# Optimization experiments

Hardware: AMD Instinct MI355X
Metric: run time of the kernel (lower is better)

## Reference

```python
import jax, jax.numpy as jnp
import numpy as np
import math

B, S, DIM, H = 4, 1024, 4096, 32
HD = DIM // H  # head_dim = 128
MAX_B, MAX_S = 4, 1024
START_POS = 0
ROPE_THETA = 10000.0


def setup_inputs() -> dict:
    key = jax.random.key(0)
    ks = jax.random.split(key, 6)
    x = jax.random.normal(ks[0], (B, S, DIM), dtype=jnp.float32)
    # real RoPE frequencies: freqs_cis[t, j] = exp(i * t * theta^{-2j/hd})
    inv_freq = 1.0 / (ROPE_THETA ** (jnp.arange(0, HD, 2, dtype=jnp.float32) / HD))  # [HD/2]
    t = jnp.arange(START_POS, START_POS + S, dtype=jnp.float32)
    ang = jnp.outer(t, inv_freq)  # [S, HD/2]
    freqs_cos = jnp.cos(ang)
    freqs_sin = jnp.sin(ang)
    # additive causal mask as in llama: -inf above diagonal offset start_pos+1
    mask = jnp.triu(jnp.full((1, 1, S, S), float('-inf'), dtype=jnp.float32), k=START_POS + 1)
    scale = 0.02
    wq = jax.random.normal(ks[1], (DIM, DIM), dtype=jnp.float32) * scale
    wk = jax.random.normal(ks[2], (DIM, DIM), dtype=jnp.float32) * scale
    wv = jax.random.normal(ks[3], (DIM, DIM), dtype=jnp.float32) * scale
    wo = jax.random.normal(ks[4], (DIM, DIM), dtype=jnp.float32) * scale
    cache_k = jnp.zeros((MAX_B, MAX_S, H, HD), dtype=jnp.float32)
    cache_v = jnp.zeros((MAX_B, MAX_S, H, HD), dtype=jnp.float32)
    return {"x": x, "start_pos": START_POS, "freqs_cos": freqs_cos, "freqs_sin": freqs_sin,
            "mask": mask, "wq": wq, "wk": wk, "wv": wv, "wo": wo,
            "cache_k": cache_k, "cache_v": cache_v}


def _apply_rotary(t, cos, sin):
    # t: [B, S, H, HD]; interpret last dim as HD/2 complex pairs (real, imag)
    b, s, h, d = t.shape
    tr = t.reshape(b, s, h, d // 2, 2)
    a, bb = tr[..., 0], tr[..., 1]
    c = cos[None, :, None, :]  # [1, S, 1, HD/2]
    si = sin[None, :, None, :]
    out_r = a * c - bb * si
    out_i = a * si + bb * c
    return jnp.stack([out_r, out_i], axis=-1).reshape(b, s, h, d)


def reference(x, start_pos, freqs_cos, freqs_sin, mask, wq, wk, wv, wo, cache_k, cache_v):
    bsz, seqlen, dim = x.shape
    hd = HD
    # torch Linear: y = x @ W.T, W is [out, in]
    xq = (x @ wq.T).reshape(bsz, seqlen, H, hd)
    xk = (x @ wk.T).reshape(bsz, seqlen, H, hd)
    xv = (x @ wv.T).reshape(bsz, seqlen, H, hd)
    xq = _apply_rotary(xq, freqs_cos, freqs_sin)
    xk = _apply_rotary(xk, freqs_cos, freqs_sin)
    # KV-cache write
    cache_k = jax.lax.dynamic_update_slice(cache_k, xk, (0, start_pos, 0, 0))
    cache_v = jax.lax.dynamic_update_slice(cache_v, xv, (0, start_pos, 0, 0))
    keys = cache_k[:bsz, :start_pos + seqlen]    # [B, K, H, HD]
    values = cache_v[:bsz, :start_pos + seqlen]  # [B, K, H, HD]
    # naive attention: full score matrix
    scores = jnp.einsum('bqhd,bkhd->bhqk', xq, keys) / math.sqrt(hd)
    scores = scores + mask
    probs = jax.nn.softmax(scores.astype(jnp.float32), axis=-1).astype(xq.dtype)
    out = jnp.einsum('bhqk,bkhd->bqhd', probs, values)
    out = out.reshape(bsz, seqlen, -1)
    return out @ wo.T
```

## Files before the change

### kernel.cpp

```cpp
#include <hip/hip_runtime.h>
#include <hip/hip_bf16.h>
#include <cstdint>

typedef __hip_bfloat16 bf16;
typedef __attribute__((ext_vector_type(8))) short frag8;
typedef __attribute__((ext_vector_type(4))) float f32x4;

#define DEV __device__ __forceinline__

DEV void gl_lds16(const void* g, void* l) {
  __builtin_amdgcn_global_load_lds(
      (const __attribute__((address_space(1))) void*)g,
      (__attribute__((address_space(3))) void*)l, 16, 0, 0);
}

DEV void storeC(float* C, size_t idx, float v) { C[idx] = v; }
DEV void storeC(bf16* C, size_t idx, float v) { C[idx] = __float2bfloat16(v); }

__global__ __launch_bounds__(256) void conv_kernel(const float* __restrict__ in,
                                                   bf16* __restrict__ out, int n8) {
  int i = blockIdx.x * 256 + threadIdx.x;
  if (i >= n8) return;
  const float4* in4 = reinterpret_cast<const float4*>(in);
  float4 a = in4[2 * i], b = in4[2 * i + 1];
  union { frag8 v; bf16 h[8]; } u;
  u.h[0] = __float2bfloat16(a.x); u.h[1] = __float2bfloat16(a.y);
  u.h[2] = __float2bfloat16(a.z); u.h[3] = __float2bfloat16(a.w);
  u.h[4] = __float2bfloat16(b.x); u.h[5] = __float2bfloat16(b.y);
  u.h[6] = __float2bfloat16(b.z); u.h[7] = __float2bfloat16(b.w);
  *reinterpret_cast<frag8*>(out + (size_t)i * 8) = u.v;
}

#define MF(a, b, c) __builtin_amdgcn_mfma_f32_16x16x32_bf16(a, b, c, 0, 0, 0)

#define STAGE(isB, h, tt, bp) do {                                             \
    char* _d = lds + ((isB) * 65536) + ((((bp) * 2) + (h)) << 14);             \
    gl_lds16(((isB) ? gB : gA)[h][0] + (size_t)(tt) * 64, _d + ldsOff0);       \
    gl_lds16(((isB) ? gB : gA)[h][1] + (size_t)(tt) * 64, _d + ldsOff1);       \
  } while (0)

#define RDA(mi, ckk) (*(const frag8*)(ab + aRowB + (mi) * 2048 + (ckk)))
#define RDB(ni, ckk) (*(const frag8*)(bb + bRowB + (ni) * 2048 + (ckk)))

#define PHASE(p, SSTAGE, SWAIT) do {                                           \
    if ((p) == 0) {                                                            \
      b00 = RDB(0, ck0); b01 = RDB(0, ck1); b10 = RDB(1, ck0); b11 = RDB(1, ck1); \
      b20 = RDB(2, ck0); b21 = RDB(2, ck1); b30 = RDB(3, ck0); b31 = RDB(3, ck1); \
    }                                                                          \
    frag8 a00 = RDA(2 * (p), ck0), a01 = RDA(2 * (p), ck1);                    \
    frag8 a10 = RDA(2 * (p) + 1, ck0), a11 = RDA(2 * (p) + 1, ck1);            \
    SSTAGE;                                                                    \
    SWAIT;                                                                     \
    __builtin_amdgcn_s_barrier();                                              \
    __builtin_amdgcn_s_setprio(1);                                             \
    acc[2*(p)][0]   = MF(a00, b00, acc[2*(p)][0]);                             \
    acc[2*(p)][1]   = MF(a00, b10, acc[2*(p)][1]);                             \
    acc[2*(p)][2]   = MF(a00, b20, acc[2*(p)][2]);                             \
    acc[2*(p)][3]   = MF(a00, b30, acc[2*(p)][3]);                             \
    acc[2*(p)+1][0] = MF(a10, b00, acc[2*(p)+1][0]);                           \
    acc[2*(p)+1][1] = MF(a10, b10, acc[2*(p)+1][1]);                           \
    acc[2*(p)+1][2] = MF(a10, b20, acc[2*(p)+1][2]);                           \
    acc[2*(p)+1][3] = MF(a10, b30, acc[2*(p)+1][3]);                           \
    acc[2*(p)][0]   = MF(a01, b01, acc[2*(p)][0]);                             \
    acc[2*(p)][1]   = MF(a01, b11, acc[2*(p)][1]);                             \
    acc[2*(p)][2]   = MF(a01, b21, acc[2*(p)][2]);                             \
    acc[2*(p)][3]   = MF(a01, b31, acc[2*(p)][3]);                             \
    acc[2*(p)+1][0] = MF(a11, b01, acc[2*(p)+1][0]);                           \
    acc[2*(p)+1][1] = MF(a11, b11, acc[2*(p)+1][1]);                           \
    acc[2*(p)+1][2] = MF(a11, b21, acc[2*(p)+1][2]);                           \
    acc[2*(p)+1][3] = MF(a11, b31, acc[2*(p)+1][3]);                           \
    __builtin_amdgcn_s_setprio(0);                                             \
    __builtin_amdgcn_s_barrier();                                              \
  } while (0)

#define VM4 asm volatile("s_waitcnt vmcnt(4)" ::: "memory")
#define VM0 asm volatile("s_waitcnt vmcnt(0)" ::: "memory")
#define NOW ((void)0)

#define TILE(t, SA, SB, SWAIT) do {                                            \
    const int _bp2 = ((t) & 1) * 2;                                            \
    char* ab = lds + ((_bp2 + wm) << 14);                                      \
    char* bb = lds + 65536 + ((_bp2 + bhalf) << 14);                           \
    PHASE(0, { if (SA) STAGE(0, 0, (t) + 1, ((t) + 1) & 1); }, NOW);           \
    PHASE(1, { if (SA) STAGE(0, 1, (t) + 1, ((t) + 1) & 1); }, NOW);           \
    PHASE(2, { if (SB) STAGE(1, 0, (t) + 2, (t) & 1); }, NOW);                 \
    PHASE(3, { if (SB) STAGE(1, 1, (t) + 2, (t) & 1); }, SWAIT);               \
  } while (0)

template <typename OutT>
__global__ __launch_bounds__(512, 2) void gemm8(const bf16* __restrict__ A,
                                                const bf16* __restrict__ Bt,
                                                OutT* __restrict__ C) {
  __shared__ __align__(16) char lds[131072];
  const int K = 4096, N = 4096;
  const int t = threadIdx.x;
  const int lane = t & 63, w = t >> 6;
  const int wm = w >> 2, wn = w & 3;
  const int lr = lane & 15, lg = lane >> 4;
  const int bhalf = wn >> 1;

  const int bid = blockIdx.x;
  const int wg = (bid & 7) * 32 + (bid >> 3);
  const int m0 = (wg >> 4) * 256, n0 = (wg & 15) * 256;

  const bf16* gA[2][2];
  const bf16* gB[2][2];
  int ldsOff0, ldsOff1;
  {
    int c0 = (w * 2 + 0) * 64 + lane;
    int c1 = (w * 2 + 1) * 64 + lane;
    int r0 = c0 >> 3, r1 = c1 >> 3;
    int e0 = ((c0 & 7) ^ (r0 & 7)) * 8;
    int e1 = ((c1 & 7) ^ (r1 & 7)) * 8;
    ldsOff0 = c0 * 16; ldsOff1 = c1 * 16;
    gA[0][0] = A + (size_t)(m0 + r0) * K + e0;
    gA[0][1] = A + (size_t)(m0 + r1) * K + e1;
    gA[1][0] = A + (size_t)(m0 + 128 + r0) * K + e0;
    gA[1][1] = A + (size_t)(m0 + 128 + r1) * K + e1;
    gB[0][0] = Bt + (size_t)(n0 + r0) * K + e0;
    gB[0][1] = Bt + (size_t)(n0 + r1) * K + e1;
    gB[1][0] = Bt + (size_t)(n0 + 128 + r0) * K + e0;
    gB[1][1] = Bt + (size_t)(n0 + 128 + r1) * K + e1;
  }

  const int swz = (lr & 7) << 4;
  const int ck0 = (lg * 16) ^ swz;
  const int ck1 = (64 + lg * 16) ^ swz;
  const int aRowB = lr * 128;
  const int bRowB = ((wn & 1) * 64 + lr) * 128;

  f32x4 acc[8][4];
#pragma unroll
  for (int mi = 0; mi < 8; ++mi)
#pragma unroll
    for (int ni = 0; ni < 4; ++ni) acc[mi][ni] = (f32x4){0.f, 0.f, 0.f, 0.f};

  frag8 b00, b01, b10, b11, b20, b21, b30, b31;

  STAGE(1, 0, 0, 0); STAGE(1, 1, 0, 0);
  STAGE(0, 0, 0, 0); STAGE(0, 1, 0, 0);
  STAGE(1, 0, 1, 1); STAGE(1, 1, 1, 1);
  VM4;
  __builtin_amdgcn_s_barrier();

  for (int tt = 0; tt < 62; tt += 2) {
    TILE(tt, 1, 1, VM4);
    TILE(tt + 1, 1, 1, VM4);
  }
  TILE(62, 1, 0, VM0);
  TILE(63, 0, 0, NOW);

#pragma unroll
  for (int mi = 0; mi < 8; ++mi)
#pragma unroll
    for (int ni = 0; ni < 4; ++ni) {
      f32x4 v = acc[mi][ni];
      int col = n0 + wn * 64 + ni * 16 + lr;
#pragma unroll
      for (int i = 0; i < 4; ++i) {
        int row = m0 + wm * 128 + mi * 16 + lg * 4 + i;
        storeC(C, (size_t)row * N + col, v[i]);
      }
    }
}

__global__ __launch_bounds__(256) void rope_kernel(bf16* __restrict__ q, bf16* __restrict__ k,
                                                   const float* __restrict__ fc,
                                                   const float* __restrict__ fs) {
  int idx = blockIdx.x * 256 + threadIdx.x;
  int i = idx & 63;
  int s = (idx >> 11) & 1023;
  float c = fc[s * 64 + i], sn = fs[s * 64 + i];
  uint32_t* qp = reinterpret_cast<uint32_t*>(q) + idx;
  uint32_t* kp = reinterpret_cast<uint32_t*>(k) + idx;
  union { uint32_t u; bf16 h[2]; } a, r;
  a.u = *qp;
  {
    float x = __bfloat162float(a.h[0]), y = __bfloat162float(a.h[1]);
    r.h[0] = __float2bfloat16(x * c - y * sn);
    r.h[1] = __float2bfloat16(x * sn + y * c);
    *qp = r.u;
  }
  a.u = *kp;
  {
    float x = __bfloat162float(a.h[0]), y = __bfloat162float(a.h[1]);
    r.h[0] = __float2bfloat16(x * c - y * sn);
    r.h[1] = __float2bfloat16(x * sn + y * c);
    *kp = r.u;
  }
}

__global__ __launch_bounds__(256) void transpose_v_kernel(const bf16* __restrict__ v,
                                                          bf16* __restrict__ vt) {
  __shared__ unsigned short tile[32][40];
  const int st = blockIdx.x * 32;
  const int dt = blockIdx.y * 32;
  const int bh = blockIdx.z;
  const int b = bh >> 5, h = bh & 31;
  const int t = threadIdx.x;
  const int r = t >> 3, c4 = (t & 7) * 4;
  const unsigned short* src = reinterpret_cast<const unsigned short*>(v) +
      ((size_t)(b * 1024 + st + r)) * 4096 + h * 128 + dt + c4;
  uint2 d = *reinterpret_cast<const uint2*>(src);
  tile[r][c4 + 0] = (unsigned short)(d.x & 0xffff);
  tile[r][c4 + 1] = (unsigned short)(d.x >> 16);
  tile[r][c4 + 2] = (unsigned short)(d.y & 0xffff);
  tile[r][c4 + 3] = (unsigned short)(d.y >> 16);
  __syncthreads();
  uint2 o;
  o.x = (uint32_t)tile[c4 + 0][r] | ((uint32_t)tile[c4 + 1][r] << 16);
  o.y = (uint32_t)tile[c4 + 2][r] | ((uint32_t)tile[c4 + 3][r] << 16);
  unsigned short* dst = reinterpret_cast<unsigned short*>(vt) +
      ((size_t)bh * 128 + dt + r) * 1024 + st + c4;
  *reinterpret_cast<uint2*>(dst) = o;
}

__global__ __launch_bounds__(256) void attn_kernel(const bf16* __restrict__ q,
                                                   const bf16* __restrict__ k,
                                                   const bf16* __restrict__ vt,
                                                   bf16* __restrict__ out) {
  __shared__ bf16 Kls[64 * 128];
  __shared__ bf16 Vls[128 * 64];
  __shared__ bf16 Pls[4][16 * 64];
  const int qt = blockIdx.x, h = blockIdx.y, b = blockIdx.z;
  const int t = threadIdx.x;
  const int lane = t & 63, wid = t >> 6;
  const int lr = lane & 15, lg = lane >> 4;

  frag8 aq[4];
  {
    const bf16* qp = q + ((size_t)(b * 1024 + qt * 64 + wid * 16 + lr)) * 4096 + h * 128 + lg * 8;
#pragma unroll
    for (int ks = 0; ks < 4; ++ks) aq[ks] = *reinterpret_cast<const frag8*>(qp + ks * 32);
  }

  const bf16* kbase = k + (size_t)b * 1024 * 4096 + h * 128;
  const bf16* vbase = vt + ((size_t)(b * 32 + h)) * 128 * 1024;
  const bf16* ksrc[4]; const bf16* vsrc[4]; char* kdst[4]; char* vdst[4];
#pragma unroll
  for (int c = 0; c < 4; ++c) {
    int L = t * 16 + c * 4096;
    int kr = L >> 8, kc = (L & 255) ^ ((kr & 7) << 4);
    ksrc[c] = kbase + (size_t)kr * 4096 + (kc >> 1);
    kdst[c] = (char*)Kls + L;
    int vr = L >> 7, vc = (L & 127) ^ ((vr & 7) << 4);
    vsrc[c] = vbase + (size_t)vr * 1024 + (vc >> 1);
    vdst[c] = (char*)Vls + L;
  }

  f32x4 oacc[8] = {};
  float mrow[4] = {-1e30f, -1e30f, -1e30f, -1e30f};
  float lrow[4] = {0.f, 0.f, 0.f, 0.f};
  char* Pw = (char*)&Pls[wid][0];
  const float scale = 0.08838834764831845f;

  for (int kt = 0; kt <= qt; ++kt) {
    __syncthreads();
#pragma unroll
    for (int c = 0; c < 4; ++c) {
      gl_lds16(ksrc[c] + (size_t)kt * 262144, kdst[c]);
      gl_lds16(vsrc[c] + kt * 64, vdst[c]);
    }
    __syncthreads();

    f32x4 sacc[4] = {};
#pragma unroll
    for (int ks = 0; ks < 4; ++ks) {
#pragma unroll
      for (int ni = 0; ni < 4; ++ni) {
        int n = ni * 16 + lr;
        frag8 bk = *reinterpret_cast<const frag8*>(
            (const char*)Kls + n * 256 + ((ks * 64 + lg * 16) ^ ((n & 7) << 4)));
        sacc[ni] = __builtin_amdgcn_mfma_f32_16x16x32_bf16(aq[ks], bk, sacc[ni], 0, 0, 0);
      }
    }

    float sv[4][4];
#pragma unroll
    for (int ni = 0; ni < 4; ++ni)
#pragma unroll
      for (int i = 0; i < 4; ++i) {
        float x = sacc[ni][i] * scale;
        if (kt == qt) {
          int qr = wid * 16 + lg * 4 + i;
          int kc = ni * 16 + lr;
          if (kc > qr) x = -1e30f;
        }
        sv[ni][i] = x;
      }

    float fs_[4];
#pragma unroll
    for (int i = 0; i < 4; ++i) {
      float pm = fmaxf(fmaxf(sv[0][i], sv[1][i]), fmaxf(sv[2][i], sv[3][i]));
#pragma unroll
      for (int m = 1; m <= 8; m <<= 1) pm = fmaxf(pm, __shfl_xor(pm, m));
      float mn = fmaxf(mrow[i], pm);
      float f = __expf(mrow[i] - mn);
      float rs = 0.f;
#pragma unroll
      for (int ni = 0; ni < 4; ++ni) {
        float p = __expf(sv[ni][i] - mn);
        sv[ni][i] = p;
        rs += p;
      }
#pragma unroll
      for (int m = 1; m <= 8; m <<= 1) rs += __shfl_xor(rs, m);
      lrow[i] = lrow[i] * f + rs;
      mrow[i] = mn;
      fs_[i] = f;
    }
#pragma unroll
    for (int nj = 0; nj < 8; ++nj)
#pragma unroll
      for (int i = 0; i < 4; ++i) oacc[nj][i] *= fs_[i];

#pragma unroll
    for (int ni = 0; ni < 4; ++ni)
#pragma unroll
      for (int i = 0; i < 4; ++i) {
        int prow = lg * 4 + i;
        int pb = prow * 128 + (((ni * 16 + lr) * 2) ^ ((prow & 7) << 4));
        *reinterpret_cast<bf16*>(Pw + pb) = __float2bfloat16(sv[ni][i]);
      }

#pragma unroll
    for (int ks2 = 0; ks2 < 2; ++ks2) {
      frag8 ap = *reinterpret_cast<const frag8*>(
          Pw + lr * 128 + ((ks2 * 64 + lg * 16) ^ ((lr & 7) << 4)));
#pragma unroll
      for (int nj = 0; nj < 8; ++nj) {
        int d = nj * 16 + lr;
        frag8 bv = *reinterpret_cast<const frag8*>(
            (const char*)Vls + d * 128 + ((ks2 * 64 + lg * 16) ^ ((d & 7) << 4)));
        oacc[nj] = __builtin_amdgcn_mfma_f32_16x16x32_bf16(ap, bv, oacc[nj], 0, 0, 0);
      }
    }
  }

#pragma unroll
  for (int nj = 0; nj < 8; ++nj)
#pragma unroll
    for (int i = 0; i < 4; ++i) {
      int srow = qt * 64 + wid * 16 + lg * 4 + i;
      out[((size_t)(b * 1024 + srow)) * 4096 + h * 128 + nj * 16 + lr] =
          __float2bfloat16(oacc[nj][i] / lrow[i]);
    }
}

extern "C" void kernel_launch(void* const* d_in, const int* in_sizes, int n_in,
                              void* d_out, int out_size, void* d_ws, size_t ws_size,
                              hipStream_t stream) {
  const float* x  = (const float*)d_in[0];
  const float* fc = (const float*)d_in[2];
  const float* fs = (const float*)d_in[3];
  const float* wq = (const float*)d_in[5];
  const float* wk = (const float*)d_in[6];
  const float* wv = (const float*)d_in[7];
  const float* wo = (const float*)d_in[8];
  float* out = (float*)d_out;

  const size_t SZ = (size_t)4096 * 4096 * 2;
  char* w = (char*)d_ws;
  bf16* xb = (bf16*)(w);
  bf16* wb = (bf16*)(w + SZ);
  bf16* qb = (bf16*)(w + 2 * SZ);
  bf16* kb = (bf16*)(w + 3 * SZ);
  bf16* vb = (bf16*)(w + 4 * SZ);
  bf16* vtb = xb;
  bf16* ao  = vb;

  const int n8 = 4096 * 4096 / 8;
  dim3 cgrd(n8 / 256), blk(256);
  dim3 ggrd(256);
  dim3 gblk(512);

  conv_kernel<<<cgrd, blk, 0, stream>>>(x, xb, n8);
  conv_kernel<<<cgrd, blk, 0, stream>>>(wq, wb, n8);
  gemm8<bf16><<<ggrd, gblk, 0, stream>>>(xb, wb, qb);
  conv_kernel<<<cgrd, blk, 0, stream>>>(wk, wb, n8);
  gemm8<bf16><<<ggrd, gblk, 0, stream>>>(xb, wb, kb);
  conv_kernel<<<cgrd, blk, 0, stream>>>(wv, wb, n8);
  gemm8<bf16><<<ggrd, gblk, 0, stream>>>(xb, wb, vb);
  rope_kernel<<<dim3(32768), blk, 0, stream>>>(qb, kb, fc, fs);
  transpose_v_kernel<<<dim3(32, 4, 128), blk, 0, stream>>>(vb, vtb);
  attn_kernel<<<dim3(16, 32, 4), blk, 0, stream>>>(qb, kb, vtb, ao);
  conv_kernel<<<cgrd, blk, 0, stream>>>(wo, wb, n8);
  gemm8<float><<<ggrd, gblk, 0, stream>>>(ao, wb, out);
}
```

Before: 749.3 us.

## Double-buffer K/V tiles in attention with 128-row query blocks of 8 waves

The attention kernel now processes 128 query rows per block with 8 waves, sharing each staged K/V tile across twice as many rows. K and V tiles are double-buffered in LDS and prefetched two tiles ahead, with the waits split by vmcnt so loads overlap MFMA work. Waves whose rows lie entirely above a causal tile skip compute, and s_setprio is raised around the MFMA loops. The cost is a larger LDS footprint and a heavier per-block causal imbalance, and the code relies on VM4/VM0/MF macros defined elsewhere.

```diff
diff --git a/kernel.cpp b/kernel.cpp
--- a/kernel.cpp
+++ b/kernel.cpp
@@ -215,137 +215,158 @@
   *reinterpret_cast<uint2*>(dst) = o;
 }
 
-__global__ __launch_bounds__(256) void attn_kernel(const bf16* __restrict__ q,
-                                                   const bf16* __restrict__ k,
-                                                   const bf16* __restrict__ vt,
-                                                   bf16* __restrict__ out) {
-  __shared__ bf16 Kls[64 * 128];
-  __shared__ bf16 Vls[128 * 64];
-  __shared__ bf16 Pls[4][16 * 64];
+__global__ __launch_bounds__(512, 4) void attn_kernel(const bf16* __restrict__ q,
+                                                      const bf16* __restrict__ k,
+                                                      const bf16* __restrict__ vt,
+                                                      bf16* __restrict__ out) {
+  __shared__ __align__(16) char als[81920];
   const int qt = blockIdx.x, h = blockIdx.y, b = blockIdx.z;
   const int t = threadIdx.x;
-  const int lane = t & 63, wid = t >> 6;
+  const int lane = t & 63, w = t >> 6;
   const int lr = lane & 15, lg = lane >> 4;
+  const int NT = 2 * qt + 2;
 
   frag8 aq[4];
   {
-    const bf16* qp = q + ((size_t)(b * 1024 + qt * 64 + wid * 16 + lr)) * 4096 + h * 128 + lg * 8;
+    const bf16* qp = q + ((size_t)(b * 1024 + qt * 128 + w * 16 + lr)) * 4096 + h * 128 + lg * 8;
 #pragma unroll
     for (int ks = 0; ks < 4; ++ks) aq[ks] = *reinterpret_cast<const frag8*>(qp + ks * 32);
   }
 
   const bf16* kbase = k + (size_t)b * 1024 * 4096 + h * 128;
   const bf16* vbase = vt + ((size_t)(b * 32 + h)) * 128 * 1024;
-  const bf16* ksrc[4]; const bf16* vsrc[4]; char* kdst[4]; char* vdst[4];
-#pragma unroll
-  for (int c = 0; c < 4; ++c) {
-    int L = t * 16 + c * 4096;
-    int kr = L >> 8, kc = (L & 255) ^ ((kr & 7) << 4);
-    ksrc[c] = kbase + (size_t)kr * 4096 + (kc >> 1);
-    kdst[c] = (char*)Kls + L;
-    int vr = L >> 7, vc = (L & 127) ^ ((vr & 7) << 4);
-    vsrc[c] = vbase + (size_t)vr * 1024 + (vc >> 1);
-    vdst[c] = (char*)Vls + L;
-  }
+
+  const int L0 = t * 16, L1 = (t + 512) * 16;
+  const int kr0 = L0 >> 8, kr1 = L1 >> 8;
+  const size_t kOff0 = (size_t)kr0 * 4096 + (((L0 & 255) ^ ((kr0 & 7) << 4)) >> 1);
+  const size_t kOff1 = (size_t)kr1 * 4096 + (((L1 & 255) ^ ((kr1 & 7) << 4)) >> 1);
+  const int vr0 = L0 >> 7, vr1 = L1 >> 7;
+  const size_t vOff0 = (size_t)vr0 * 1024 + (((L0 & 127) ^ ((vr0 & 7) << 4)) >> 1);
+  const size_t vOff1 = (size_t)vr1 * 1024 + (((L1 & 127) ^ ((vr1 & 7) << 4)) >> 1);
+
+#define STAGE_K(tt, bp) do { char* _d = als + (bp) * 16384;                    \
+    gl_lds16(kbase + (size_t)(tt) * 262144 + kOff0, _d + L0);                  \
+    gl_lds16(kbase + (size_t)(tt) * 262144 + kOff1, _d + L1); } while (0)
+#define STAGE_V(tt, bp) do { char* _d = als + 32768 + (bp) * 16384;            \
+    gl_lds16(vbase + (size_t)(tt) * 64 + vOff0, _d + L0);                      \
+    gl_lds16(vbase + (size_t)(tt) * 64 + vOff1, _d + L1); } while (0)
 
   f32x4 oacc[8] = {};
   float mrow[4] = {-1e30f, -1e30f, -1e30f, -1e30f};
   float lrow[4] = {0.f, 0.f, 0.f, 0.f};
-  char* Pw = (char*)&Pls[wid][0];
+  char* Pw = als + 65536 + w * 2048;
   const float scale = 0.08838834764831845f;
-
-  for (int kt = 0; kt <= qt; ++kt) {
-    __syncthreads();
-#pragma unroll
-    for (int c = 0; c < 4; ++c) {
-      gl_lds16(ksrc[c] + (size_t)kt * 262144, kdst[c]);
-      gl_lds16(vsrc[c] + kt * 64, vdst[c]);
+  const int qmaxw = qt * 128 + w * 16 + 15;
+
+  STAGE_K(0, 0); STAGE_V(0, 0);
+  STAGE_K(1, 1); STAGE_V(1, 1);
+
+  for (int kt = 0; kt < NT; ++kt) {
+    const int cur = kt & 1;
+    const bool act = (kt * 64 <= qmaxw);
+    const bool domask = (kt >= 2 * qt);
+    char* Kc = als + cur * 16384;
+    char* Vc = als + 32768 + cur * 16384;
+
+    if (kt + 1 < NT) { VM4; } else { VM0; }
+    __builtin_amdgcn_s_barrier();
+
+    f32x4 sacc[4] = {};
+    if (act) {
+      __builtin_amdgcn_s_setprio(1);
+#pragma unroll
+      for (int ks = 0; ks < 4; ++ks) {
+#pragma unroll
+        for (int ni = 0; ni < 4; ++ni) {
+          int n = ni * 16 + lr;
+          frag8 bk = *reinterpret_cast<const frag8*>(
+              Kc + n * 256 + ((ks * 64 + lg * 16) ^ ((n & 7) << 4)));
+          sacc[ni] = MF(aq[ks], bk, sacc[ni]);
+        }
+      }
+      __builtin_amdgcn_s_setprio(0);
     }
-    __syncthreads();
-
-    f32x4 sacc[4] = {};
-#pragma unroll
-    for (int ks = 0; ks < 4; ++ks) {
-#pragma unroll
-      for (int ni = 0; ni < 4; ++ni) {
-        int n = ni * 16 + lr;
-        frag8 bk = *reinterpret_cast<const frag8*>(
-            (const char*)Kls + n * 256 + ((ks * 64 + lg * 16) ^ ((n & 7) << 4)));
-        sacc[ni] = __builtin_amdgcn_mfma_f32_16x16x32_bf16(aq[ks], bk, sacc[ni], 0, 0, 0);
+    __builtin_amdgcn_s_barrier();
+    if (kt + 2 < NT) STAGE_K(kt + 2, cur);
+
+    if (act) {
+#pragma unroll
+      for (int ni = 0; ni < 4; ++ni)
+#pragma unroll
+        for (int i = 0; i < 4; ++i) {
+          float x = sacc[ni][i] * scale;
+          if (domask) {
+            int qr = qt * 128 + w * 16 + lg * 4 + i;
+            int kc = kt * 64 + ni * 16 + lr;
+            if (kc > qr) x = -1e30f;
+          }
+          sacc[ni][i] = x;
+        }
+
+      float fs_[4];
+#pragma unroll
+      for (int i = 0; i < 4; ++i) {
+        float pm = fmaxf(fmaxf(sacc[0][i], sacc[1][i]), fmaxf(sacc[2][i], sacc[3][i]));
+#pragma unroll
+        for (int m = 1; m <= 8; m <<= 1) pm = fmaxf(pm, __shfl_xor(pm, m));
+        float mn = fmaxf(mrow[i], pm);
+        float f = __expf(mrow[i] - mn);
+        float rs = 0.f;
+#pragma unroll
+        for (int ni = 0; ni < 4; ++ni) {
+          float p = __expf(sacc[ni][i] - mn);
+          sacc[ni][i] = p;
+          rs += p;
+        }
+#pragma unroll
+        for (int m = 1; m <= 8; m <<= 1) rs += __shfl_xor(rs, m);
+        lrow[i] = lrow[i] * f + rs;
+        mrow[i] = mn;
+        fs_[i] = f;
       }
+#pragma unroll
+      for (int nj = 0; nj < 8; ++nj)
+#pragma unroll
+        for (int i = 0; i < 4; ++i) oacc[nj][i] *= fs_[i];
+
+#pragma unroll
+      for (int ni = 0; ni < 4; ++ni)
+#pragma unroll
+        for (int i = 0; i < 4; ++i) {
+          int prow = lg * 4 + i;
+          int pb = prow * 128 + (((ni * 16 + lr) * 2) ^ ((prow & 7) << 4));
+          *reinterpret_cast<bf16*>(Pw + pb) = __float2bfloat16(sacc[ni][i]);
+        }
+
+      __builtin_amdgcn_s_setprio(1);
+#pragma unroll
+      for (int ks2 = 0; ks2 < 2; ++ks2) {
+        frag8 ap = *reinterpret_cast<const frag8*>(
+            Pw + lr * 128 + ((ks2 * 64 + lg * 16) ^ ((lr & 7) << 4)));
+#pragma unroll
+        for (int nj = 0; nj < 8; ++nj) {
+          int d = nj * 16 + lr;
+          frag8 bv = *reinterpret_cast<const frag8*>(
+              Vc + d * 128 + ((ks2 * 64 + lg * 16) ^ ((d & 7) << 4)));
+          oacc[nj] = MF(ap, bv, oacc[nj]);
+        }
+      }
+      __builtin_amdgcn_s_setprio(0);
     }
-
-    float sv[4][4];
-#pragma unroll
-    for (int ni = 0; ni < 4; ++ni)
-#pragma unroll
-      for (int i = 0; i < 4; ++i) {
-        float x = sacc[ni][i] * scale;
-        if (kt == qt) {
-          int qr = wid * 16 + lg * 4 + i;
-          int kc = ni * 16 + lr;
-          if (kc > qr) x = -1e30f;
-        }
-        sv[ni][i] = x;
-      }
-
-    float fs_[4];
+    __builtin_amdgcn_s_barrier();
+    if (kt + 2 < NT) STAGE_V(kt + 2, cur);
+  }
+
+#pragma unroll
+  for (int nj = 0; nj < 8; ++nj)
 #pragma unroll
     for (int i = 0; i < 4; ++i) {
-      float pm = fmaxf(fmaxf(sv[0][i], sv[1][i]), fmaxf(sv[2][i], sv[3][i]));
-#pragma unroll
-      for (int m = 1; m <= 8; m <<= 1) pm = fmaxf(pm, __shfl_xor(pm, m));
-      float mn = fmaxf(mrow[i], pm);
-      float f = __expf(mrow[i] - mn);
-      float rs = 0.f;
-#pragma unroll
-      for (int ni = 0; ni < 4; ++ni) {
-        float p = __expf(sv[ni][i] - mn);
-        sv[ni][i] = p;
-        rs += p;
-      }
-#pragma unroll
-      for (int m = 1; m <= 8; m <<= 1) rs += __shfl_xor(rs, m);
-      lrow[i] = lrow[i] * f + rs;
-      mrow[i] = mn;
-      fs_[i] = f;
-    }
-#pragma unroll
-    for (int nj = 0; nj < 8; ++nj)
-#pragma unroll
-      for (int i = 0; i < 4; ++i) oacc[nj][i] *= fs_[i];
-
-#pragma unroll
-    for (int ni = 0; ni < 4; ++ni)
-#pragma unroll
-      for (int i = 0; i < 4; ++i) {
-        int prow = lg * 4 + i;
-        int pb = prow * 128 + (((ni * 16 + lr) * 2) ^ ((prow & 7) << 4));
-        *reinterpret_cast<bf16*>(Pw + pb) = __float2bfloat16(sv[ni][i]);
-      }
-
-#pragma unroll
-    for (int ks2 = 0; ks2 < 2; ++ks2) {
-      frag8 ap = *reinterpret_cast<const frag8*>(
-          Pw + lr * 128 + ((ks2 * 64 + lg * 16) ^ ((lr & 7) << 4)));
-#pragma unroll
-      for (int nj = 0; nj < 8; ++nj) {
-        int d = nj * 16 + lr;
-        frag8 bv = *reinterpret_cast<const frag8*>(
-            (const char*)Vls + d * 128 + ((ks2 * 64 + lg * 16) ^ ((d & 7) << 4)));
-        oacc[nj] = __builtin_amdgcn_mfma_f32_16x16x32_bf16(ap, bv, oacc[nj], 0, 0, 0);
-      }
-    }
-  }
-
-#pragma unroll
-  for (int nj = 0; nj < 8; ++nj)
-#pragma unroll
-    for (int i = 0; i < 4; ++i) {
-      int srow = qt * 64 + wid * 16 + lg * 4 + i;
+      int srow = qt * 128 + w * 16 + lg * 4 + i;
       out[((size_t)(b * 1024 + srow)) * 4096 + h * 128 + nj * 16 + lr] =
           __float2bfloat16(oacc[nj][i] / lrow[i]);
     }
+#undef STAGE_K
+#undef STAGE_V
 }
 
 extern "C" void kernel_launch(void* const* d_in, const int* in_sizes, int n_in,
@@ -384,7 +405,7 @@
   gemm8<bf16><<<ggrd, gblk, 0, stream>>>(xb, wb, vb);
   rope_kernel<<<dim3(32768), blk, 0, stream>>>(qb, kb, fc, fs);
   transpose_v_kernel<<<dim3(32, 4, 128), blk, 0, stream>>>(vb, vtb);
-  attn_kernel<<<dim3(16, 32, 4), blk, 0, stream>>>(qb, kb, vtb, ao);
+  attn_kernel<<<dim3(8, 32, 4), gblk, 0, stream>>>(qb, kb, vtb, ao);
   conv_kernel<<<cgrd, blk, 0, stream>>>(wo, wb, n8);
   gemm8<float><<<ggrd, gblk, 0, stream>>>(ao, wb, out);
 }
```

After: 712.3 us. -4.9%, faster.
